# Performance work log

Hardware: AMD Instinct MI355X
Metric: run time of the kernel (lower is better)

Reference implementation:

```python
import jax, jax.numpy as jnp
import numpy as np

D_MODEL = 1024
N_HEADS = 16
HEAD_DIM = D_MODEL // N_HEADS
THETA = 10000.0
NEG = -1e9


def apply_rope(x, positions, theta=THETA):
    # x: (B, H, S, d), positions: (B, 1, S)
    d = x.shape[-1]
    inv_freq = 1.0 / (theta ** (jnp.arange(0, d, 2, dtype=jnp.float32) / d))  # (d/2,)
    freqs = positions[..., None].astype(jnp.float32) * inv_freq  # (B, 1, S, d/2)
    cos, sin = jnp.cos(freqs), jnp.sin(freqs)
    xr = x.reshape(x.shape[:-1] + (d // 2, 2))
    xe, xo = xr[..., 0], xr[..., 1]
    rot = jnp.stack([xe * cos - xo * sin, xe * sin + xo * cos], axis=-1)
    return rot.reshape(x.shape)


def setup_inputs() -> dict:
    key = jax.random.key(0)
    ks = jax.random.split(key, 5)
    B, S = 2, 2048
    scale = 1.0 / np.sqrt(D_MODEL)
    return {
        "x": jax.random.normal(ks[0], (B, S, D_MODEL), dtype=jnp.float32),
        "wq": jax.random.normal(ks[1], (D_MODEL, D_MODEL), dtype=jnp.float32) * scale,
        "wk": jax.random.normal(ks[2], (D_MODEL, D_MODEL), dtype=jnp.float32) * scale,
        "wv": jax.random.normal(ks[3], (D_MODEL, D_MODEL), dtype=jnp.float32) * scale,
        "wo": jax.random.normal(ks[4], (D_MODEL, D_MODEL), dtype=jnp.float32) * scale,
        "token_positions": jnp.arange(S, dtype=jnp.int64),
    }


def reference(x, wq, wk, wv, wo, token_positions):
    B, S, D = x.shape
    H, d = N_HEADS, HEAD_DIM
    # QKV projections (module does x @ w.T)
    q = (x @ wq.T).reshape(B, S, H, d).transpose(0, 2, 1, 3)  # (B, H, S, d)
    k = (x @ wk.T).reshape(B, S, H, d).transpose(0, 2, 1, 3)
    v = (x @ wv.T).reshape(B, S, H, d).transpose(0, 2, 1, 3)
    pos = jnp.broadcast_to(token_positions[None, :], (B, S))[:, None, :]  # (B, 1, S)
    q = apply_rope(q, pos)
    k = apply_rope(k, pos)
    scores = jnp.einsum("bhqd,bhkd->bhqk", q, k) / jnp.sqrt(jnp.float32(d))
    causal = jnp.tril(jnp.ones((S, S), dtype=bool))
    scores = jnp.where(causal[None, None], scores, NEG)
    attn = jax.nn.softmax(scores, axis=-1)
    out = jnp.einsum("bhqk,bhkd->bhqd", attn, v)
    out = out.transpose(0, 2, 1, 3).reshape(B, S, D)
    return out @ wo.T
```

## Files before the change

### kernel.cpp

```cpp
#include <hip/hip_runtime.h>

typedef __bf16 bf16;
typedef __bf16 bf16x8 __attribute__((ext_vector_type(8)));
typedef __bf16 bf16x4 __attribute__((ext_vector_type(4)));
typedef float f32x4 __attribute__((ext_vector_type(4)));
typedef float f32x16 __attribute__((ext_vector_type(16)));
typedef float fx2 __attribute__((ext_vector_type(2)));

#define DEV static __device__ __forceinline__

constexpr int BB = 2, SS = 2048, DM = 1024, NH = 16, HD = 64;
constexpr int MTOT = BB * SS;
constexpr float LOG2E = 1.4426950408889634f;

constexpr size_t OFF_XB   = 0;
constexpr size_t OFF_WQKV = OFF_XB   + (size_t)MTOT * DM * 2;
constexpr size_t OFF_WO   = OFF_WQKV + (size_t)3 * DM * DM * 2;
constexpr size_t OFF_TAB  = OFF_WO   + (size_t)DM * DM * 2;
constexpr size_t OFF_Q    = OFF_TAB  + (size_t)SS * (HD/2) * 8;
constexpr size_t OFF_KF   = OFF_Q    + (size_t)MTOT * DM * 2;
constexpr size_t OFF_VF   = OFF_KF   + (size_t)MTOT * DM * 2;
constexpr size_t OFF_AO   = OFF_VF   + (size_t)MTOT * DM * 2;

typedef const __attribute__((address_space(1))) void gas_void;
typedef __attribute__((address_space(3))) void las_void;

DEV void gload16(const bf16* g, bf16* l) {
  __builtin_amdgcn_global_load_lds((gas_void*)g, (las_void*)l, 16, 0, 0);
}

DEV f32x4 mfma16(bf16x8 a, bf16x8 b, f32x4 c) {
  return __builtin_amdgcn_mfma_f32_16x16x32_bf16(a, b, c, 0, 0, 0);
}

DEV f32x16 mfma32(bf16x8 a, bf16x8 b, f32x16 c) {
  return __builtin_amdgcn_mfma_f32_32x32x16_bf16(a, b, c, 0, 0, 0);
}

DEV unsigned pack2(float a, float b) {
  union { bf16 h[2]; unsigned u; } cv;
  cv.h[0] = (bf16)a; cv.h[1] = (bf16)b;
  return cv.u;
}

__global__ void prep_kernel(const float* __restrict__ x, const float* __restrict__ wq,
    const float* __restrict__ wk, const float* __restrict__ wv, const float* __restrict__ wo,
    const int* __restrict__ pos, bf16* __restrict__ xb, bf16* __restrict__ wqkv,
    bf16* __restrict__ wob, fx2* __restrict__ tab) {
  const int NX4 = MTOT * DM / 4;
  const int NW4 = DM * DM / 4;
  const int TOTC = NX4 + 4 * NW4;
  const int NTAB = SS * (HD / 2);
  const int total = TOTC + NTAB;
  for (int i = blockIdx.x * blockDim.x + threadIdx.x; i < total; i += gridDim.x * blockDim.x) {
    if (i < TOTC) {
      const float* src; bf16* dst; int off;
      if (i < NX4) { src = x; dst = xb; off = i; }
      else {
        int i2 = i - NX4; int which = i2 >> 18; off = i2 & (NW4 - 1);
        src = which == 0 ? wq : which == 1 ? wk : which == 2 ? wv : wo;
        dst = which == 0 ? wqkv : which == 1 ? wqkv + DM * DM : which == 2 ? wqkv + 2 * DM * DM : wob;
      }
      float4 v = ((const float4*)src)[off];
      bf16x4 o4 = { (bf16)v.x, (bf16)v.y, (bf16)v.z, (bf16)v.w };
      ((bf16x4*)dst)[off] = o4;
    } else {
      int e = i - TOTC;
      int s = e >> 5, p = e & 31;
      float invf = __builtin_exp2f(-(float)p * (13.287712379549449f / 32.0f));
      float ang = (float)pos[s] * invf;
      fx2 cs; cs.x = cosf(ang); cs.y = sinf(ang);
      tab[e] = cs;
    }
  }
}

DEV void gemm_bt_128(const bf16* __restrict__ A, const bf16* __restrict__ Bw,
                     int rowA0, int rowB0, f32x4 (&acc)[4][4], bf16* lds) {
  const int t = threadIdx.x, w = t >> 6, lane = t & 63;
  const int wr = w >> 1, wc = w & 1, g = lane >> 4, c = lane & 15;
#pragma unroll
  for (int mi = 0; mi < 4; mi++)
#pragma unroll
    for (int ni = 0; ni < 4; ni++) acc[mi][ni] = (f32x4){0.f, 0.f, 0.f, 0.f};
  const bf16* ga = A + (size_t)(rowA0 + (t >> 2)) * DM + (t & 3) * 8;
  const bf16* gb = Bw + (size_t)(rowB0 + (t >> 2)) * DM + (t & 3) * 8;
  const int arow = wr * 64 + c, brow = wc * 64 + c;
  auto stage = [&](int k0, int buf) {
    bf16* la = lds + buf * 8192 + w * 512;
    bf16* lb = lds + buf * 8192 + 4096 + w * 512;
    gload16(ga + k0,            la);
    gload16(ga + k0 + 64 * DM,  la + 2048);
    gload16(gb + k0,            lb);
    gload16(gb + k0 + 64 * DM,  lb + 2048);
  };
  stage(0, 0);
  stage(32, 1);
  asm volatile("s_waitcnt vmcnt(4)" ::: "memory");
  __builtin_amdgcn_s_barrier();
  __builtin_amdgcn_sched_barrier(0);
  for (int it = 0; it < 32; ++it) {
    const int cur = it % 3;
    const bf16* lA = lds + cur * 8192;
    const bf16* lB = lds + cur * 8192 + 4096;
    bf16x8 af[4], bf_[4];
#pragma unroll
    for (int mi = 0; mi < 4; mi++) af[mi]  = *(const bf16x8*)(lA + (arow + mi * 16) * 32 + g * 8);
#pragma unroll
    for (int ni = 0; ni < 4; ni++) bf_[ni] = *(const bf16x8*)(lB + (brow + ni * 16) * 32 + g * 8);
#pragma unroll
    for (int mi = 0; mi < 4; mi++)
#pragma unroll
      for (int ni = 0; ni < 4; ni++)
        acc[mi][ni] = mfma16(af[mi], bf_[ni], acc[mi][ni]);
    if (it + 2 < 32) stage((it + 2) * 32, (it + 2) % 3);
    if (it + 1 < 32) {
      if (it + 2 < 32) asm volatile("s_waitcnt vmcnt(4)" ::: "memory");
      else             asm volatile("s_waitcnt vmcnt(0)" ::: "memory");
      __builtin_amdgcn_s_barrier();
      __builtin_amdgcn_sched_barrier(0);
    }
  }
}

__global__ __launch_bounds__(256, 3) void qkv_kernel(const bf16* __restrict__ xb,
    const bf16* __restrict__ wqkv, const fx2* __restrict__ tab,
    bf16* __restrict__ Qb, bf16* __restrict__ KFb, bf16* __restrict__ VFb) {
  __shared__ __align__(16) bf16 L[24576];
  f32x4 acc[4][4];
  const int rowA0 = blockIdx.y * 128, rowB0 = blockIdx.x * 128;
  gemm_bt_128(xb, wqkv, rowA0, rowB0, acc, L);
  const int t = threadIdx.x, w = t >> 6, lane = t & 63;
  const int wr = w >> 1, wc = w & 1, g = lane >> 4, c = lane & 15;
  const int which = rowB0 >> 10;
  const int b = rowA0 >> 11;
  const int s0 = rowA0 & (SS - 1);
  const int h0 = (rowB0 & (DM - 1)) >> 6;
  const int kt0 = s0 >> 6;
#pragma unroll
  for (int mi = 0; mi < 4; mi++)
#pragma unroll
    for (int ni = 0; ni < 4; ni++) {
      const int col = wc * 64 + ni * 16 + c;
      const int hh = col >> 6, dd = col & 63;
#pragma unroll
      for (int j = 0; j < 4; j++) {
        const int sp = wr * 64 + mi * 16 + 4 * g + j;
        float v = acc[mi][ni][j];
        int flat;
        if (which < 2) {
          const int s = s0 + sp;
          float partner = __shfl_xor(v, 1);
          fx2 cs = tab[s * 32 + (dd >> 1)];
          v = v * cs.x + ((dd & 1) ? partner : -partner) * cs.y;
          if (which == 0) {
            flat = hh * 8192 + sp * 64 + dd;
          } else {
            const int spp = sp & 63;
            flat = (hh * 2 + (sp >> 6)) * 4096 +
                   (((spp >> 5) * 4 + (dd >> 4)) * 64 + (spp & 31) + 32 * ((dd >> 3) & 1)) * 8 +
                   (dd & 7);
          }
        } else {
          const int spp = sp & 63;
          flat = (hh * 2 + (sp >> 6)) * 4096 +
                 (((dd >> 5) * 4 + mi) * 64 + (dd & 31) + 32 * (g >> 1)) * 8 + (spp & 7);
        }
        L[flat] = (bf16)v;
      }
    }
  __syncthreads();
  if (which == 0) {
    bf16* base0 = Qb + ((size_t)(b * NH + h0) * SS + s0) * HD;
    bf16* base1 = Qb + ((size_t)(b * NH + h0 + 1) * SS + s0) * HD;
#pragma unroll
    for (int j2 = 0; j2 < 8; j2++) {
      const int off = j2 * 2048 + t * 8;
      bf16* dst = (off < 8192 ? base0 : base1) + (off & 8191);
      *(bf16x8*)dst = *(const bf16x8*)(L + off);
    }
  } else {
    bf16* outp = (which == 1) ? KFb : VFb;
#pragma unroll
    for (int j2 = 0; j2 < 8; j2++) {
      const int off = j2 * 2048 + t * 8;
      const int r = off >> 12;
      bf16* dst = outp + ((size_t)(b * NH + h0 + (r >> 1)) * 32 + kt0 + (r & 1)) * 4096 + (off & 4095);
      *(bf16x8*)dst = *(const bf16x8*)(L + off);
    }
  }
}

__global__ __launch_bounds__(256, 4) void attn_kernel(const bf16* __restrict__ Q,
    const bf16* __restrict__ KF, const bf16* __restrict__ VF, bf16* __restrict__ AO) {
  __shared__ float Om[3][2048];
  __shared__ float Ml[3][32];
  __shared__ float Ll[3][32];
  const int flat = blockIdx.x;
  const int flat2 = (flat & 7) * 128 + (flat >> 3);
  const int bh = flat2 >> 5;
  const int p = flat2 & 31;
  const int w = threadIdx.x >> 6;
  const int lane = threadIdx.x & 63;
  const int q31 = lane & 31, hi = lane >> 5;
  const bf16* Qp = Q + (size_t)bh * SS * HD;
  const bf16* KFp = KF + (size_t)bh * SS * HD;
  const bf16* VFp = VF + (size_t)bh * SS * HD;
  const float SCL = 0.125f * LOG2E;

  auto run_chunk = [&](int qbase, int nt) {
    bf16x8 qb[4];
#pragma unroll
    for (int ds = 0; ds < 4; ds++) {
      bf16x8 xq = *(const bf16x8*)(Qp + (size_t)(qbase + q31) * HD + ds * 16 + hi * 8);
#pragma unroll
      for (int e = 0; e < 8; e++) xq[e] = (bf16)((float)xq[e] * SCL);
      qb[ds] = xq;
    }
    float m_r = -3.0e38f, lsum = 0.f;
    f32x16 o0, o1;
#pragma unroll
    for (int e = 0; e < 16; e++) { o0[e] = 0.f; o1[e] = 0.f; }

    for (int tv = w; tv < nt; tv += 4) {
      const int k0 = tv * 64;
      const bf16* kt = KFp + (size_t)tv * 4096;
      const bf16* vt = VFp + (size_t)tv * 4096;
      f32x16 s0, s1;
#pragma unroll
      for (int e = 0; e < 16; e++) { s0[e] = 0.f; s1[e] = 0.f; }
      {
        bf16x8 kf[4];
#pragma unroll
        for (int ds = 0; ds < 4; ds++)
          kf[ds] = *(const bf16x8*)(kt + (size_t)(ds * 64 + lane) * 8);
#pragma unroll
        for (int ds = 0; ds < 4; ds++) s0 = mfma32(kf[ds], qb[ds], s0);
#pragma unroll
        for (int ds = 0; ds < 4; ds++)
          kf[ds] = *(const bf16x8*)(kt + (size_t)((4 + ds) * 64 + lane) * 8);
#pragma unroll
        for (int ds = 0; ds < 4; ds++) s1 = mfma32(kf[ds], qb[ds], s1);
      }
      if (k0 + 63 > qbase) {
        const int qg = qbase + q31;
#pragma unroll
        for (int r = 0; r < 16; r++) {
          const int kg = k0 + (r & 3) + 8 * (r >> 2) + 4 * hi;
          if (kg > qg)      s0[r] = -1.0e30f;
          if (kg + 32 > qg) s1[r] = -1.0e30f;
        }
      }
      {
        float a[16];
#pragma unroll
        for (int r = 0; r < 16; r++) a[r] = fmaxf(s0[r], s1[r]);
#pragma unroll
        for (int d = 8; d > 0; d >>= 1)
#pragma unroll
          for (int r = 0; r < d; r++) a[r] = fmaxf(a[r], a[r + d]);
        const float pm = fmaxf(a[0], __shfl_xor(a[0], 32));
        if (__any(pm > m_r + 8.0f)) {
          const float mnew = fmaxf(m_r, pm);
          const float alpha = __builtin_exp2f(m_r - mnew);
          lsum *= alpha;
#pragma unroll
          for (int e = 0; e < 16; e++) { o0[e] *= alpha; o1[e] *= alpha; }
          m_r = mnew;
        }
        float b[16];
#pragma unroll
        for (int r = 0; r < 16; r++) {
          s0[r] = __builtin_exp2f(s0[r] - m_r);
          s1[r] = __builtin_exp2f(s1[r] - m_r);
          b[r] = s0[r] + s1[r];
        }
#pragma unroll
        for (int d = 8; d > 0; d >>= 1)
#pragma unroll
          for (int r = 0; r < d; r++) b[r] += b[r + d];
        lsum += b[0] + __shfl_xor(b[0], 32);
      }
      bf16x8 pf[4];
#pragma unroll
      for (int ks = 0; ks < 4; ks++) {
        const int rb = 8 * (ks & 1);
        float va0, va1, va2, va3, vb0, vb1, vb2, vb3;
        if (ks < 2) {
          va0 = s0[rb]; va1 = s0[rb + 1]; va2 = s0[rb + 2]; va3 = s0[rb + 3];
          vb0 = s0[rb + 4]; vb1 = s0[rb + 5]; vb2 = s0[rb + 6]; vb3 = s0[rb + 7];
        } else {
          va0 = s1[rb]; va1 = s1[rb + 1]; va2 = s1[rb + 2]; va3 = s1[rb + 3];
          vb0 = s1[rb + 4]; vb1 = s1[rb + 5]; vb2 = s1[rb + 6]; vb3 = s1[rb + 7];
        }
        const unsigned a01 = pack2(va0, va1), a23 = pack2(va2, va3);
        const unsigned b01 = pack2(vb0, vb1), b23 = pack2(vb2, vb3);
        const unsigned z1 = (unsigned)__shfl_xor((int)(hi ? a01 : b01), 32);
        const unsigned z2 = (unsigned)__shfl_xor((int)(hi ? a23 : b23), 32);
        union { unsigned u[4]; bf16x8 v; } cv;
        cv.u[0] = hi ? z1 : a01;
        cv.u[1] = hi ? z2 : a23;
        cv.u[2] = hi ? b01 : z1;
        cv.u[3] = hi ? b23 : z2;
        pf[ks] = cv.v;
      }
      {
        bf16x8 vf[4];
#pragma unroll
        for (int ks = 0; ks < 4; ks++)
          vf[ks] = *(const bf16x8*)(vt + (size_t)(ks * 64 + lane) * 8);
#pragma unroll
        for (int ks = 0; ks < 4; ks++) o0 = mfma32(vf[ks], pf[ks], o0);
#pragma unroll
        for (int ks = 0; ks < 4; ks++)
          vf[ks] = *(const bf16x8*)(vt + (size_t)((4 + ks) * 64 + lane) * 8);
#pragma unroll
        for (int ks = 0; ks < 4; ks++) o1 = mfma32(vf[ks], pf[ks], o1);
      }
    }
    __syncthreads();
    if (w) {
#pragma unroll
      for (int e = 0; e < 16; e++) {
        const int r = (e & 3) + 8 * (e >> 2) + 4 * hi;
        Om[w - 1][r * 32 + q31] = o0[e];
        Om[w - 1][(r + 32) * 32 + q31] = o1[e];
      }
      if (!hi) { Ml[w - 1][q31] = m_r; Ll[w - 1][q31] = lsum; }
    }
    __syncthreads();
    if (!w) {
      float mi_[3];
#pragma unroll
      for (int i = 0; i < 3; i++) mi_[i] = Ml[i][q31];
      float mm = fmaxf(fmaxf(m_r, mi_[0]), fmaxf(mi_[1], mi_[2]));
      const float aS = __builtin_exp2f(m_r - mm);
      float ai[3];
      float L2 = aS * lsum;
#pragma unroll
      for (int i = 0; i < 3; i++) {
        ai[i] = __builtin_exp2f(mi_[i] - mm);
        L2 += ai[i] * Ll[i][q31];
      }
      const float linv = 1.0f / L2;
      const int b = bh >> 4, h = bh & 15;
      const size_t rowb = ((size_t)(b * SS + qbase + q31)) * DM + h * HD;
#pragma unroll
      for (int g2 = 0; g2 < 4; g2++) {
        bf16x4 w0v, w1v;
#pragma unroll
        for (int j = 0; j < 4; j++) {
          const int e = 4 * g2 + j;
          const int r = j + 8 * g2 + 4 * hi;
          float v0 = aS * o0[e];
          float v1 = aS * o1[e];
#pragma unroll
          for (int i = 0; i < 3; i++) {
            v0 += ai[i] * Om[i][r * 32 + q31];
            v1 += ai[i] * Om[i][(r + 32) * 32 + q31];
          }
          w0v[j] = (bf16)(v0 * linv);
          w1v[j] = (bf16)(v1 * linv);
        }
        *(bf16x4*)(AO + rowb +      8 * g2 + 4 * hi) = w0v;
        *(bf16x4*)(AO + rowb + 32 + 8 * g2 + 4 * hi) = w1v;
      }
    }
    __syncthreads();
  };

  run_chunk(p * 32, p / 2 + 1);
  const int ph = 63 - p;
  run_chunk(ph * 32, ph / 2 + 1);
}

__global__ __launch_bounds__(256, 2) void oproj_kernel(const bf16* __restrict__ AO,
    const bf16* __restrict__ wob, float* __restrict__ out) {
  __shared__ __align__(16) bf16 L[24576];
  f32x4 acc[4][4];
  const int rowA0 = blockIdx.y * 128, rowB0 = blockIdx.x * 128;
  gemm_bt_128(AO, wob, rowA0, rowB0, acc, L);
  const int t = threadIdx.x, w = t >> 6, lane = t & 63;
  const int wr = w >> 1, wc = w & 1, g = lane >> 4, c = lane & 15;
#pragma unroll
  for (int mi = 0; mi < 4; mi++)
#pragma unroll
    for (int ni = 0; ni < 4; ni++) {
      const int ncol = rowB0 + wc * 64 + ni * 16 + c;
#pragma unroll
      for (int j = 0; j < 4; j++) {
        const int mrow = rowA0 + wr * 64 + mi * 16 + 4 * g + j;
        out[(size_t)mrow * DM + ncol] = acc[mi][ni][j];
      }
    }
}

extern "C" void kernel_launch(void* const* d_in, const int* in_sizes, int n_in,
                              void* d_out, int out_size, void* d_ws, size_t ws_size,
                              hipStream_t stream) {
  const float* x  = (const float*)d_in[0];
  const float* wq = (const float*)d_in[1];
  const float* wk = (const float*)d_in[2];
  const float* wv = (const float*)d_in[3];
  const float* wo = (const float*)d_in[4];
  const int*   pos = (const int*)d_in[5];
  char* ws = (char*)d_ws;
  bf16* xb   = (bf16*)(ws + OFF_XB);
  bf16* wqkv = (bf16*)(ws + OFF_WQKV);
  bf16* wob  = (bf16*)(ws + OFF_WO);
  fx2*  tab  = (fx2*)(ws + OFF_TAB);
  bf16* Qb   = (bf16*)(ws + OFF_Q);
  bf16* KFb  = (bf16*)(ws + OFF_KF);
  bf16* VFb  = (bf16*)(ws + OFF_VF);
  bf16* AOb  = (bf16*)(ws + OFF_AO);

  hipLaunchKernelGGL(prep_kernel, dim3(2048), dim3(256), 0, stream,
                     x, wq, wk, wv, wo, pos, xb, wqkv, wob, tab);
  hipLaunchKernelGGL(qkv_kernel, dim3(24, 32), dim3(256), 0, stream,
                     xb, wqkv, tab, Qb, KFb, VFb);
  hipLaunchKernelGGL(attn_kernel, dim3(1024), dim3(256), 0, stream,
                     Qb, KFb, VFb, AOb);
  hipLaunchKernelGGL(oproj_kernel, dim3(8, 32), dim3(256), 0, stream,
                     AOb, wob, (float*)d_out);
}
```

Measured before the change: 118.2 us.

## Process both batch heads per attention block to interleave two independent softmax chains

Each attention block now handles the same head for both batch elements, running two independent QK/softmax/PV chains in one loop iteration. The grid is halved and launch bounds drop to 2 waves per SIMD, and the causal-pair chunk order is reversed so the long chunk runs first. The aim is more instruction-level parallelism per wave and shared mask and loop overhead, at the cost of doubled register and LDS use and fewer resident blocks.

New measurement: 128.0 us. 8.3% more time.

```diff
diff --git a/kernel.cpp b/kernel.cpp
--- a/kernel.cpp
+++ b/kernel.cpp
@@ -191,107 +191,135 @@
   }
 }
 
-__global__ __launch_bounds__(256, 4) void attn_kernel(const bf16* __restrict__ Q,
+__global__ __launch_bounds__(256, 2) void attn_kernel(const bf16* __restrict__ Q,
     const bf16* __restrict__ KF, const bf16* __restrict__ VF, bf16* __restrict__ AO) {
-  __shared__ float Om[3][2048];
-  __shared__ float Ml[3][32];
-  __shared__ float Ll[3][32];
+  __shared__ float OmA[3][2048], OmB[3][2048];
+  __shared__ float MlA[3][32], LlA[3][32], MlB[3][32], LlB[3][32];
   const int flat = blockIdx.x;
-  const int flat2 = (flat & 7) * 128 + (flat >> 3);
-  const int bh = flat2 >> 5;
-  const int p = flat2 & 31;
+  const int flat2 = (flat & 7) * 64 + (flat >> 3);
+  const int h = flat2 >> 5;
+  const int pi = flat2 & 31;
   const int w = threadIdx.x >> 6;
   const int lane = threadIdx.x & 63;
   const int q31 = lane & 31, hi = lane >> 5;
-  const bf16* Qp = Q + (size_t)bh * SS * HD;
-  const bf16* KFp = KF + (size_t)bh * SS * HD;
-  const bf16* VFp = VF + (size_t)bh * SS * HD;
+  const int bh0 = h, bh1 = NH + h;
+  const bf16* QpA = Q + (size_t)bh0 * SS * HD;
+  const bf16* QpB = Q + (size_t)bh1 * SS * HD;
+  const bf16* KFpA = KF + (size_t)bh0 * SS * HD;
+  const bf16* KFpB = KF + (size_t)bh1 * SS * HD;
+  const bf16* VFpA = VF + (size_t)bh0 * SS * HD;
+  const bf16* VFpB = VF + (size_t)bh1 * SS * HD;
   const float SCL = 0.125f * LOG2E;
 
-  auto run_chunk = [&](int qbase, int nt) {
-    bf16x8 qb[4];
+  auto run_dual = [&](int ci) {
+    const int qbase = ci * 32;
+    const int nt = ci / 2 + 1;
+    bf16x8 qbA[4], qbB[4];
 #pragma unroll
     for (int ds = 0; ds < 4; ds++) {
-      bf16x8 xq = *(const bf16x8*)(Qp + (size_t)(qbase + q31) * HD + ds * 16 + hi * 8);
-#pragma unroll
-      for (int e = 0; e < 8; e++) xq[e] = (bf16)((float)xq[e] * SCL);
-      qb[ds] = xq;
-    }
-    float m_r = -3.0e38f, lsum = 0.f;
-    f32x16 o0, o1;
-#pragma unroll
-    for (int e = 0; e < 16; e++) { o0[e] = 0.f; o1[e] = 0.f; }
+      bf16x8 xa = *(const bf16x8*)(QpA + (size_t)(qbase + q31) * HD + ds * 16 + hi * 8);
+      bf16x8 xb2 = *(const bf16x8*)(QpB + (size_t)(qbase + q31) * HD + ds * 16 + hi * 8);
+#pragma unroll
+      for (int e = 0; e < 8; e++) {
+        xa[e]  = (bf16)((float)xa[e]  * SCL);
+        xb2[e] = (bf16)((float)xb2[e] * SCL);
+      }
+      qbA[ds] = xa; qbB[ds] = xb2;
+    }
+    float mA = -3.0e38f, lA = 0.f, mB = -3.0e38f, lB = 0.f;
+    f32x16 oA0, oA1, oB0, oB1;
+#pragma unroll
+    for (int e = 0; e < 16; e++) { oA0[e] = 0.f; oA1[e] = 0.f; oB0[e] = 0.f; oB1[e] = 0.f; }
 
     for (int tv = w; tv < nt; tv += 4) {
       const int k0 = tv * 64;
-      const bf16* kt = KFp + (size_t)tv * 4096;
-      const bf16* vt = VFp + (size_t)tv * 4096;
-      f32x16 s0, s1;
-#pragma unroll
-      for (int e = 0; e < 16; e++) { s0[e] = 0.f; s1[e] = 0.f; }
+      const bf16* ktA = KFpA + (size_t)tv * 4096;
+      const bf16* ktB = KFpB + (size_t)tv * 4096;
+      const bf16* vtA = VFpA + (size_t)tv * 4096;
+      const bf16* vtB = VFpB + (size_t)tv * 4096;
+      const bool diag = (k0 + 63 > qbase);
+      const int qg = qbase + q31;
+      f32x16 sA0, sA1;
+#pragma unroll
+      for (int e = 0; e < 16; e++) { sA0[e] = 0.f; sA1[e] = 0.f; }
       {
         bf16x8 kf[4];
 #pragma unroll
         for (int ds = 0; ds < 4; ds++)
-          kf[ds] = *(const bf16x8*)(kt + (size_t)(ds * 64 + lane) * 8);
-#pragma unroll
-        for (int ds = 0; ds < 4; ds++) s0 = mfma32(kf[ds], qb[ds], s0);
+          kf[ds] = *(const bf16x8*)(ktA + (size_t)(ds * 64 + lane) * 8);
+#pragma unroll
+        for (int ds = 0; ds < 4; ds++) sA0 = mfma32(kf[ds], qbA[ds], sA0);
 #pragma unroll
         for (int ds = 0; ds < 4; ds++)
-          kf[ds] = *(const bf16x8*)(kt + (size_t)((4 + ds) * 64 + lane) * 8);
-#pragma unroll
-        for (int ds = 0; ds < 4; ds++) s1 = mfma32(kf[ds], qb[ds], s1);
-      }
-      if (k0 + 63 > qbase) {
-        const int qg = qbase + q31;
+          kf[ds] = *(const bf16x8*)(ktA + (size_t)((4 + ds) * 64 + lane) * 8);
+#pragma unroll
+        for (int ds = 0; ds < 4; ds++) sA1 = mfma32(kf[ds], qbA[ds], sA1);
+      }
+      f32x16 sB0, sB1;
+#pragma unroll
+      for (int e = 0; e < 16; e++) { sB0[e] = 0.f; sB1[e] = 0.f; }
+      {
+        bf16x8 kf[4];
+#pragma unroll
+        for (int ds = 0; ds < 4; ds++)
+          kf[ds] = *(const bf16x8*)(ktB + (size_t)(ds * 64 + lane) * 8);
+#pragma unroll
+        for (int ds = 0; ds < 4; ds++) sB0 = mfma32(kf[ds], qbB[ds], sB0);
+#pragma unroll
+        for (int ds = 0; ds < 4; ds++)
+          kf[ds] = *(const bf16x8*)(ktB + (size_t)((4 + ds) * 64 + lane) * 8);
+#pragma unroll
+        for (int ds = 0; ds < 4; ds++) sB1 = mfma32(kf[ds], qbB[ds], sB1);
+      }
+      if (diag) {
 #pragma unroll
         for (int r = 0; r < 16; r++) {
           const int kg = k0 + (r & 3) + 8 * (r >> 2) + 4 * hi;
-          if (kg > qg)      s0[r] = -1.0e30f;
-          if (kg + 32 > qg) s1[r] = -1.0e30f;
+          if (kg > qg)      { sA0[r] = -1.0e30f; sB0[r] = -1.0e30f; }
+          if (kg + 32 > qg) { sA1[r] = -1.0e30f; sB1[r] = -1.0e30f; }
         }
       }
       {
         float a[16];
 #pragma unroll
-        for (int r = 0; r < 16; r++) a[r] = fmaxf(s0[r], s1[r]);
+        for (int r = 0; r < 16; r++) a[r] = fmaxf(sA0[r], sA1[r]);
 #pragma unroll
         for (int d = 8; d > 0; d >>= 1)
 #pragma unroll
           for (int r = 0; r < d; r++) a[r] = fmaxf(a[r], a[r + d]);
         const float pm = fmaxf(a[0], __shfl_xor(a[0], 32));
-        if (__any(pm > m_r + 8.0f)) {
-          const float mnew = fmaxf(m_r, pm);
-          const float alpha = __builtin_exp2f(m_r - mnew);
-          lsum *= alpha;
-#pragma unroll
-          for (int e = 0; e < 16; e++) { o0[e] *= alpha; o1[e] *= alpha; }
-          m_r = mnew;
-        }
-        float b[16];
+        if (__any(pm > mA + 8.0f)) {
+          const float mnew = fmaxf(mA, pm);
+          const float alpha = __builtin_exp2f(mA - mnew);
+          lA *= alpha;
+#pragma unroll
+          for (int e = 0; e < 16; e++) { oA0[e] *= alpha; oA1[e] *= alpha; }
+          mA = mnew;
+        }
+        float b2[16];
 #pragma unroll
         for (int r = 0; r < 16; r++) {
-          s0[r] = __builtin_exp2f(s0[r] - m_r);
-          s1[r] = __builtin_exp2f(s1[r] - m_r);
-          b[r] = s0[r] + s1[r];
+          sA0[r] = __builtin_exp2f(sA0[r] - mA);
+          sA1[r] = __builtin_exp2f(sA1[r] - mA);
+          b2[r] = sA0[r] + sA1[r];
         }
 #pragma unroll
         for (int d = 8; d > 0; d >>= 1)
 #pragma unroll
-          for (int r = 0; r < d; r++) b[r] += b[r + d];
-        lsum += b[0] + __shfl_xor(b[0], 32);
-      }
-      bf16x8 pf[4];
+          for (int r = 0; r < d; r++) b2[r] += b2[r + d];
+        lA += b2[0] + __shfl_xor(b2[0], 32);
+      }
+      bf16x8 pfA[4];
 #pragma unroll
       for (int ks = 0; ks < 4; ks++) {
         const int rb = 8 * (ks & 1);
         float va0, va1, va2, va3, vb0, vb1, vb2, vb3;
         if (ks < 2) {
-          va0 = s0[rb]; va1 = s0[rb + 1]; va2 = s0[rb + 2]; va3 = s0[rb + 3];
-          vb0 = s0[rb + 4]; vb1 = s0[rb + 5]; vb2 = s0[rb + 6]; vb3 = s0[rb + 7];
+          va0 = sA0[rb]; va1 = sA0[rb + 1]; va2 = sA0[rb + 2]; va3 = sA0[rb + 3];
+          vb0 = sA0[rb + 4]; vb1 = sA0[rb + 5]; vb2 = sA0[rb + 6]; vb3 = sA0[rb + 7];
         } else {
-          va0 = s1[rb]; va1 = s1[rb + 1]; va2 = s1[rb + 2]; va3 = s1[rb + 3];
-          vb0 = s1[rb + 4]; vb1 = s1[rb + 5]; vb2 = s1[rb + 6]; vb3 = s1[rb + 7];
+          va0 = sA1[rb]; va1 = sA1[rb + 1]; va2 = sA1[rb + 2]; va3 = sA1[rb + 3];
+          vb0 = sA1[rb + 4]; vb1 = sA1[rb + 5]; vb2 = sA1[rb + 6]; vb3 = sA1[rb + 7];
         }
         const unsigned a01 = pack2(va0, va1), a23 = pack2(va2, va3);
         const unsigned b01 = pack2(vb0, vb1), b23 = pack2(vb2, vb3);
@@ -302,20 +330,86 @@
         cv.u[1] = hi ? z2 : a23;
         cv.u[2] = hi ? b01 : z1;
         cv.u[3] = hi ? b23 : z2;
-        pf[ks] = cv.v;
+        pfA[ks] = cv.v;
       }
       {
         bf16x8 vf[4];
 #pragma unroll
         for (int ks = 0; ks < 4; ks++)
-          vf[ks] = *(const bf16x8*)(vt + (size_t)(ks * 64 + lane) * 8);
-#pragma unroll
-        for (int ks = 0; ks < 4; ks++) o0 = mfma32(vf[ks], pf[ks], o0);
+          vf[ks] = *(const bf16x8*)(vtA + (size_t)(ks * 64 + lane) * 8);
+#pragma unroll
+        for (int ks = 0; ks < 4; ks++) oA0 = mfma32(vf[ks], pfA[ks], oA0);
 #pragma unroll
         for (int ks = 0; ks < 4; ks++)
-          vf[ks] = *(const bf16x8*)(vt + (size_t)((4 + ks) * 64 + lane) * 8);
-#pragma unroll
-        for (int ks = 0; ks < 4; ks++) o1 = mfma32(vf[ks], pf[ks], o1);
+          vf[ks] = *(const bf16x8*)(vtA + (size_t)((4 + ks) * 64 + lane) * 8);
+#pragma unroll
+        for (int ks = 0; ks < 4; ks++) oA1 = mfma32(vf[ks], pfA[ks], oA1);
+      }
+      {
+        float a[16];
+#pragma unroll
+        for (int r = 0; r < 16; r++) a[r] = fmaxf(sB0[r], sB1[r]);
+#pragma unroll
+        for (int d = 8; d > 0; d >>= 1)
+#pragma unroll
+          for (int r = 0; r < d; r++) a[r] = fmaxf(a[r], a[r + d]);
+        const float pm = fmaxf(a[0], __shfl_xor(a[0], 32));
+        if (__any(pm > mB + 8.0f)) {
+          const float mnew = fmaxf(mB, pm);
+          const float alpha = __builtin_exp2f(mB - mnew);
+          lB *= alpha;
+#pragma unroll
+          for (int e = 0; e < 16; e++) { oB0[e] *= alpha; oB1[e] *= alpha; }
+          mB = mnew;
+        }
+        float b2[16];
+#pragma unroll
+        for (int r = 0; r < 16; r++) {
+          sB0[r] = __builtin_exp2f(sB0[r] - mB);
+          sB1[r] = __builtin_exp2f(sB1[r] - mB);
+          b2[r] = sB0[r] + sB1[r];
+        }
+#pragma unroll
+        for (int d = 8; d > 0; d >>= 1)
+#pragma unroll
+          for (int r = 0; r < d; r++) b2[r] += b2[r + d];
+        lB += b2[0] + __shfl_xor(b2[0], 32);
+      }
+      bf16x8 pfB[4];
+#pragma unroll
+      for (int ks = 0; ks < 4; ks++) {
+        const int rb = 8 * (ks & 1);
+        float va0, va1, va2, va3, vb0, vb1, vb2, vb3;
+        if (ks < 2) {
+          va0 = sB0[rb]; va1 = sB0[rb + 1]; va2 = sB0[rb + 2]; va3 = sB0[rb + 3];
+          vb0 = sB0[rb + 4]; vb1 = sB0[rb + 5]; vb2 = sB0[rb + 6]; vb3 = sB0[rb + 7];
+        } else {
+          va0 = sB1[rb]; va1 = sB1[rb + 1]; va2 = sB1[rb + 2]; va3 = sB1[rb + 3];
+          vb0 = sB1[rb + 4]; vb1 = sB1[rb + 5]; vb2 = sB1[rb + 6]; vb3 = sB1[rb + 7];
+        }
+        const unsigned a01 = pack2(va0, va1), a23 = pack2(va2, va3);
+        const unsigned b01 = pack2(vb0, vb1), b23 = pack2(vb2, vb3);
+        const unsigned z1 = (unsigned)__shfl_xor((int)(hi ? a01 : b01), 32);
+        const unsigned z2 = (unsigned)__shfl_xor((int)(hi ? a23 : b23), 32);
+        union { unsigned u[4]; bf16x8 v; } cv;
+        cv.u[0] = hi ? z1 : a01;
+        cv.u[1] = hi ? z2 : a23;
+        cv.u[2] = hi ? b01 : z1;
+        cv.u[3] = hi ? b23 : z2;
+        pfB[ks] = cv.v;
+      }
+      {
+        bf16x8 vf[4];
+#pragma unroll
+        for (int ks = 0; ks < 4; ks++)
+          vf[ks] = *(const bf16x8*)(vtB + (size_t)(ks * 64 + lane) * 8);
+#pragma unroll
+        for (int ks = 0; ks < 4; ks++) oB0 = mfma32(vf[ks], pfB[ks], oB0);
+#pragma unroll
+        for (int ks = 0; ks < 4; ks++)
+          vf[ks] = *(const bf16x8*)(vtB + (size_t)((4 + ks) * 64 + lane) * 8);
+#pragma unroll
+        for (int ks = 0; ks < 4; ks++) oB1 = mfma32(vf[ks], pfB[ks], oB1);
       }
     }
     __syncthreads();
@@ -323,55 +417,68 @@
 #pragma unroll
       for (int e = 0; e < 16; e++) {
         const int r = (e & 3) + 8 * (e >> 2) + 4 * hi;
-        Om[w - 1][r * 32 + q31] = o0[e];
-        Om[w - 1][(r + 32) * 32 + q31] = o1[e];
-      }
-      if (!hi) { Ml[w - 1][q31] = m_r; Ll[w - 1][q31] = lsum; }
+        OmA[w - 1][r * 32 + q31] = oA0[e];
+        OmA[w - 1][(r + 32) * 32 + q31] = oA1[e];
+        OmB[w - 1][r * 32 + q31] = oB0[e];
+        OmB[w - 1][(r + 32) * 32 + q31] = oB1[e];
+      }
+      if (!hi) {
+        MlA[w - 1][q31] = mA; LlA[w - 1][q31] = lA;
+        MlB[w - 1][q31] = mB; LlB[w - 1][q31] = lB;
+      }
     }
     __syncthreads();
     if (!w) {
-      float mi_[3];
-#pragma unroll
-      for (int i = 0; i < 3; i++) mi_[i] = Ml[i][q31];
-      float mm = fmaxf(fmaxf(m_r, mi_[0]), fmaxf(mi_[1], mi_[2]));
-      const float aS = __builtin_exp2f(m_r - mm);
-      float ai[3];
-      float L2 = aS * lsum;
-#pragma unroll
-      for (int i = 0; i < 3; i++) {
-        ai[i] = __builtin_exp2f(mi_[i] - mm);
-        L2 += ai[i] * Ll[i][q31];
-      }
-      const float linv = 1.0f / L2;
-      const int b = bh >> 4, h = bh & 15;
-      const size_t rowb = ((size_t)(b * SS + qbase + q31)) * DM + h * HD;
-#pragma unroll
-      for (int g2 = 0; g2 < 4; g2++) {
-        bf16x4 w0v, w1v;
-#pragma unroll
-        for (int j = 0; j < 4; j++) {
-          const int e = 4 * g2 + j;
-          const int r = j + 8 * g2 + 4 * hi;
-          float v0 = aS * o0[e];
-          float v1 = aS * o1[e];
-#pragma unroll
-          for (int i = 0; i < 3; i++) {
-            v0 += ai[i] * Om[i][r * 32 + q31];
-            v1 += ai[i] * Om[i][(r + 32) * 32 + q31];
+#pragma unroll
+      for (int cb = 0; cb < 2; cb++) {
+        float (*Om)[2048] = cb ? OmB : OmA;
+        float (*Ml)[32] = cb ? MlB : MlA;
+        float (*Ll)[32] = cb ? LlB : LlA;
+        const float mS = cb ? mB : mA;
+        const float lS = cb ? lB : lA;
+        f32x16& p0 = cb ? oB0 : oA0;
+        f32x16& p1 = cb ? oB1 : oA1;
+        float mi_[3];
+#pragma unroll
+        for (int i = 0; i < 3; i++) mi_[i] = Ml[i][q31];
+        float mm = fmaxf(fmaxf(mS, mi_[0]), fmaxf(mi_[1], mi_[2]));
+        const float aS = __builtin_exp2f(mS - mm);
+        float ai[3];
+        float L2 = aS * lS;
+#pragma unroll
+        for (int i = 0; i < 3; i++) {
+          ai[i] = __builtin_exp2f(mi_[i] - mm);
+          L2 += ai[i] * Ll[i][q31];
+        }
+        const float linv = 1.0f / L2;
+        const size_t rowb = ((size_t)(cb * SS + qbase + q31)) * DM + h * HD;
+#pragma unroll
+        for (int g2 = 0; g2 < 4; g2++) {
+          bf16x4 w0v, w1v;
+#pragma unroll
+          for (int j = 0; j < 4; j++) {
+            const int e = 4 * g2 + j;
+            const int r = j + 8 * g2 + 4 * hi;
+            float v0 = aS * p0[e];
+            float v1 = aS * p1[e];
+#pragma unroll
+            for (int i = 0; i < 3; i++) {
+              v0 += ai[i] * Om[i][r * 32 + q31];
+              v1 += ai[i] * Om[i][(r + 32) * 32 + q31];
+            }
+            w0v[j] = (bf16)(v0 * linv);
+            w1v[j] = (bf16)(v1 * linv);
           }
-          w0v[j] = (bf16)(v0 * linv);
-          w1v[j] = (bf16)(v1 * linv);
-        }
-        *(bf16x4*)(AO + rowb +      8 * g2 + 4 * hi) = w0v;
-        *(bf16x4*)(AO + rowb + 32 + 8 * g2 + 4 * hi) = w1v;
+          *(bf16x4*)(AO + rowb +      8 * g2 + 4 * hi) = w0v;
+          *(bf16x4*)(AO + rowb + 32 + 8 * g2 + 4 * hi) = w1v;
+        }
       }
     }
     __syncthreads();
   };
 
-  run_chunk(p * 32, p / 2 + 1);
-  const int ph = 63 - p;
-  run_chunk(ph * 32, ph / 2 + 1);
+  run_dual(63 - pi);
+  run_dual(pi);
 }
 
 __global__ __launch_bounds__(256, 2) void oproj_kernel(const bf16* __restrict__ AO,
@@ -418,7 +525,7 @@
                      x, wq, wk, wv, wo, pos, xb, wqkv, wob, tab);
   hipLaunchKernelGGL(qkv_kernel, dim3(24, 32), dim3(256), 0, stream,
                      xb, wqkv, tab, Qb, KFb, VFb);
-  hipLaunchKernelGGL(attn_kernel, dim3(1024), dim3(256), 0, stream,
+  hipLaunchKernelGGL(attn_kernel, dim3(512), dim3(256), 0, stream,
                      Qb, KFb, VFb, AOb);
   hipLaunchKernelGGL(oproj_kernel, dim3(8, 32), dim3(256), 0, stream,
                      AOb, wob, (float*)d_out);
```
